# Optimization experiments

Hardware: AMD Instinct MI355X
Metric: run time of the kernel (lower is better)

## Reference

```python
import jax, jax.numpy as jnp
import numpy as np

B, S, E, H = 2, 2048, 2048, 16
D = E // H  # head_dim = 128


def setup_inputs() -> dict:
    key = jax.random.key(0)
    ks = jax.random.split(key, 11)
    scale = 1.0 / np.sqrt(E)
    return {
        "query": jax.random.normal(ks[0], (B, S, E), dtype=jnp.float32),
        "key_in": jax.random.normal(ks[1], (B, S, E), dtype=jnp.float32),
        "value": jax.random.normal(ks[2], (B, S, E), dtype=jnp.float32),
        "Wq": jax.random.normal(ks[3], (E, E), dtype=jnp.float32) * scale,
        "bq": jnp.zeros((E,), dtype=jnp.float32),
        "Wk": jax.random.normal(ks[4], (E, E), dtype=jnp.float32) * scale,
        "bk": jnp.zeros((E,), dtype=jnp.float32),
        "Wv": jax.random.normal(ks[5], (E, E), dtype=jnp.float32) * scale,
        "bv": jnp.zeros((E,), dtype=jnp.float32),
        "Wo": jax.random.normal(ks[6], (E, E), dtype=jnp.float32) * scale,
        "bo": jnp.zeros((E,), dtype=jnp.float32),
    }


def reference(query, key_in, value, Wq, bq, Wk, bk, Wv, bv, Wo, bo):
    # Linear projections then split heads: (B,S,E) -> (B,H,S,D)
    def proj(x, W, b):
        y = x @ W + b
        return y.reshape(B, S, H, D).transpose(0, 2, 1, 3)

    Q = proj(query, Wq, bq)
    K = proj(key_in, Wk, bk)
    V = proj(value, Wv, bv)

    # scores: (B,H,S,S)
    scores = jnp.einsum('bhqd,bhkd->bhqk', Q, K) / jnp.sqrt(jnp.float32(D))
    attn = jax.nn.softmax(scores, axis=-1)
    # attn output: (B,H,S,D) -> (B,S,E)
    out = jnp.einsum('bhqk,bhkd->bhqd', attn, V)
    out = out.transpose(0, 2, 1, 3).reshape(B, S, E)
    return out @ Wo + bo
```

## Files before the change

kernel.cpp:

```cpp
#include <hip/hip_runtime.h>
#include <hip/hip_bf16.h>

typedef __bf16 bf16;
typedef __bf16 bf16x8 __attribute__((ext_vector_type(8)));
typedef float f32x4 __attribute__((ext_vector_type(4)));

constexpr int kE = 2048;
constexpr int kS = 2048;
constexpr int kB = 2;
constexpr int kH = 16;
constexpr int kD = 128;
constexpr int kM = kB * kS;
constexpr float kQScale = 0.12751743f;

#define MFMA_BF16(A, B, C) __builtin_amdgcn_mfma_f32_16x16x32_bf16((A), (B), (C), 0, 0, 0)

__device__ __forceinline__ void async_ld16(const void* gsrc, void* ldst) {
  __builtin_amdgcn_global_load_lds(
      (__attribute__((address_space(1))) void*)(gsrc),
      (__attribute__((address_space(3))) void*)(ldst), 16, 0, 0);
}

__global__ __launch_bounds__(256) void cvt_kernel(
    const float* __restrict__ Xq, const float* __restrict__ Xk,
    const float* __restrict__ Xv, bf16* __restrict__ Y) {
  const int z = blockIdx.y;
  const float* X = (z == 0) ? Xq : (z == 1) ? Xk : Xv;
  bf16* Yz = Y + (size_t)z * kM * kE;
  size_t i = ((size_t)blockIdx.x * 256 + threadIdx.x) * 8;
  float4 v0 = *(const float4*)(X + i);
  float4 v1 = *(const float4*)(X + i + 4);
  bf16x8 hv;
  hv[0] = (bf16)v0.x; hv[1] = (bf16)v0.y; hv[2] = (bf16)v0.z; hv[3] = (bf16)v0.w;
  hv[4] = (bf16)v1.x; hv[5] = (bf16)v1.y; hv[6] = (bf16)v1.z; hv[7] = (bf16)v1.w;
  *(bf16x8*)(Yz + i) = hv;
}

__global__ __launch_bounds__(256) void wt_kernel(
    const float* __restrict__ Wq, const float* __restrict__ Wk,
    const float* __restrict__ Wv, const float* __restrict__ Wo,
    bf16* __restrict__ WT) {
  __shared__ bf16 tl[64][72];
  const int z = blockIdx.z;
  const float* W = (z == 0) ? Wq : (z == 1) ? Wk : (z == 2) ? Wv : Wo;
  const int n0 = blockIdx.x * 64, k0 = blockIdx.y * 64;
  const int t = threadIdx.x;

  {
    const int k = t >> 2, nq = (t & 3) * 16;
    const float* src = &W[(size_t)(k0 + k) * kE + n0 + nq];
#pragma unroll
    for (int u = 0; u < 4; ++u) {
      float4 v = *(const float4*)(src + u * 4);
      tl[nq + u * 4 + 0][k] = (bf16)v.x;
      tl[nq + u * 4 + 1][k] = (bf16)v.y;
      tl[nq + u * 4 + 2][k] = (bf16)v.z;
      tl[nq + u * 4 + 3][k] = (bf16)v.w;
    }
  }
  __syncthreads();
  {
    const int n = t >> 2, seg = (t & 3) * 16;
    bf16x8 a = *(const bf16x8*)&tl[n][seg];
    bf16x8 b2 = *(const bf16x8*)&tl[n][seg + 8];
    bf16* dst = &WT[(size_t)(z * kE + n0 + n) * kE + k0 + seg];
    *(bf16x8*)dst = a;
    *(bf16x8*)(dst + 8) = b2;
  }
}

__global__ __launch_bounds__(256) void gemm_qkv_kernel(
    const bf16* __restrict__ A, const bf16* __restrict__ Bt,
    const float* __restrict__ bias, bf16* __restrict__ dstbuf,
    const float oscale) {
  __shared__ alignas(16) bf16 As[128 * 64];
  __shared__ alignas(16) bf16 Bs[128 * 64];

  const int n0 = blockIdx.x * 128;
  const int m0 = blockIdx.y * 128;
  const int t = threadIdx.x;
  const int lane = t & 63;
  const int w = t >> 6;
  const int ln = lane & 15;
  const int qd = lane >> 4;
  const int wm = w >> 1, wn = w & 1;

  const f32x4 fzero = {0.f, 0.f, 0.f, 0.f};
  f32x4 acc[4][4];
#pragma unroll
  for (int i = 0; i < 4; ++i)
#pragma unroll
    for (int j = 0; j < 4; ++j) acc[i][j] = fzero;

  for (int k0 = 0; k0 < kE; k0 += 64) {
    __syncthreads();
#pragma unroll
    for (int i = 0; i < 4; ++i) {
      int c = t + i * 256;
      int row = c >> 3;
      int slot = c & 7;
      int g = slot ^ (row & 7);
      async_ld16(&A[(size_t)(m0 + row) * kE + k0 + g * 8],
                 &As[(size_t)(w * 64 + i * 256) * 8]);
    }
#pragma unroll
    for (int i = 0; i < 4; ++i) {
      int c = t + i * 256;
      int row = c >> 3;
      int slot = c & 7;
      int g = slot ^ (row & 7);
      async_ld16(&Bt[(size_t)(n0 + row) * kE + k0 + g * 8],
                 &Bs[(size_t)(w * 64 + i * 256) * 8]);
    }
    __syncthreads();
#pragma unroll
    for (int ks = 0; ks < 2; ++ks) {
      bf16x8 af[4], bfv[4];
#pragma unroll
      for (int i = 0; i < 4; ++i) {
        int row = wm * 64 + i * 16 + ln;
        int slot = (ks * 4 + qd) ^ (ln & 7);
        af[i] = *(const bf16x8*)&As[row * 64 + slot * 8];
      }
#pragma unroll
      for (int j = 0; j < 4; ++j) {
        int row = wn * 64 + j * 16 + ln;
        int slot = (ks * 4 + qd) ^ (ln & 7);
        bfv[j] = *(const bf16x8*)&Bs[row * 64 + slot * 8];
      }
#pragma unroll
      for (int i = 0; i < 4; ++i)
#pragma unroll
        for (int j = 0; j < 4; ++j)
          acc[i][j] = MFMA_BF16(af[i], bfv[j], acc[i][j]);
    }
  }

#pragma unroll
  for (int i = 0; i < 4; ++i) {
    int mbase = m0 + wm * 64 + i * 16 + qd * 4;
#pragma unroll
    for (int j = 0; j < 4; ++j) {
      int n = n0 + wn * 64 + j * 16 + ln;
      float bn = bias[n];
      int h = n >> 7, d = n & 127;
#pragma unroll
      for (int r = 0; r < 4; ++r) {
        int mm = mbase + r;
        int bb = mm >> 11, ss = mm & (kS - 1);
        dstbuf[((size_t)(bb * kH + h) * kS + ss) * kD + d] =
            (bf16)((acc[i][j][r] + bn) * oscale);
      }
    }
  }
}

__global__ __launch_bounds__(256) void vtrans_kernel(
    const bf16* __restrict__ Vb, bf16* __restrict__ VT) {
  __shared__ bf16 tl[64][72];
  const int bh = blockIdx.z;
  const int s0 = blockIdx.x * 64, d0 = blockIdx.y * 64;
  const bf16* src = Vb + ((size_t)bh * kS + s0) * kD + d0;
  bf16* dst = VT + ((size_t)bh * kD + d0) * kS + s0;
  const int t = threadIdx.x;
#pragma unroll
  for (int i = 0; i < 2; ++i) {
    int c = t + i * 256;
    int s = c >> 3, dc = (c & 7) * 8;
    bf16x8 v = *(const bf16x8*)&src[(size_t)s * kD + dc];
#pragma unroll
    for (int e = 0; e < 8; ++e) tl[dc + e][s] = v[e];
  }
  __syncthreads();
#pragma unroll
  for (int i = 0; i < 2; ++i) {
    int c = t + i * 256;
    int d = c >> 3, sc = (c & 7) * 8;
    bf16x8 v = *(const bf16x8*)&tl[d][sc];
    *(bf16x8*)&dst[(size_t)d * kS + sc] = v;
  }
}

__global__ __launch_bounds__(256) void attn_kernel(
    const bf16* __restrict__ Qb, const bf16* __restrict__ Kb,
    const bf16* __restrict__ VTb, bf16* __restrict__ AO) {
  __shared__ alignas(16) bf16 Kt[2][64 * 128];
  __shared__ alignas(16) bf16 Vt[2][128 * 64];
  __shared__ alignas(16) bf16 Pl[4][32 * 64];

  const int wg = blockIdx.x;
  const int swz = (wg & 7) * 64 + (wg >> 3);
  const int bh = swz >> 4;
  const int q0 = (swz & 15) * 128;
  const int t = threadIdx.x, lane = t & 63, w = t >> 6;
  const int ln = lane & 15, qd = lane >> 4;

  const bf16* Qh = Qb + (size_t)bh * kS * kD;
  const bf16* Kh = Kb + (size_t)bh * kS * kD;
  const bf16* Vh = VTb + (size_t)bh * kD * kS;

  bf16x8 qf[2][4];
#pragma unroll
  for (int m = 0; m < 2; ++m) {
    int qr = q0 + w * 32 + m * 16 + ln;
#pragma unroll
    for (int f = 0; f < 4; ++f)
      qf[m][f] = *(const bf16x8*)&Qh[(size_t)qr * kD + f * 32 + qd * 8];
  }

  auto stage = [&](int buf, int kc) {
#pragma unroll
    for (int i = 0; i < 4; ++i) {
      int c = t + i * 256;
      int row = c >> 4;
      int slot = c & 15;
      int g = slot ^ (row & 15);
      async_ld16(&Kh[(size_t)(kc + row) * kD + g * 8],
                 &Kt[buf][(size_t)(w * 64 + i * 256) * 8]);
    }
#pragma unroll
    for (int i = 0; i < 4; ++i) {
      int c = t + i * 256;
      int row = c >> 3;
      int slot = c & 7;
      int g = slot ^ (row & 7);
      async_ld16(&Vh[(size_t)row * kS + kc + g * 8],
                 &Vt[buf][(size_t)(w * 64 + i * 256) * 8]);
    }
  };

  const f32x4 fzero = {0.f, 0.f, 0.f, 0.f};
  f32x4 o[2][8];
#pragma unroll
  for (int m = 0; m < 2; ++m)
#pragma unroll
    for (int dt = 0; dt < 8; ++dt) o[m][dt] = fzero;
  float lsum[2][4] = {{0.f, 0.f, 0.f, 0.f}, {0.f, 0.f, 0.f, 0.f}};

  stage(0, 0);

#pragma unroll 1
  for (int u = 0; u < 32; ++u) {
    const int cur = u & 1;
    int knext = (u < 31) ? (u + 1) * 64 : 31 * 64;
    stage(cur ^ 1, knext);
    asm volatile("s_waitcnt vmcnt(8)" ::: "memory");
    __builtin_amdgcn_s_barrier();
    asm volatile("" ::: "memory");

    f32x4 s[2][4];
#pragma unroll
    for (int m = 0; m < 2; ++m)
#pragma unroll
      for (int nt = 0; nt < 4; ++nt) s[m][nt] = fzero;
    __builtin_amdgcn_s_setprio(1);
#pragma unroll
    for (int nt = 0; nt < 4; ++nt) {
      int row = nt * 16 + ln;
#pragma unroll
      for (int f = 0; f < 4; ++f) {
        int slot = (f * 4 + qd) ^ ln;
        bf16x8 kfv = *(const bf16x8*)&Kt[cur][row * 128 + slot * 8];
        s[0][nt] = MFMA_BF16(qf[0][f], kfv, s[0][nt]);
        s[1][nt] = MFMA_BF16(qf[1][f], kfv, s[1][nt]);
      }
    }
    __builtin_amdgcn_s_setprio(0);

#pragma unroll
    for (int m = 0; m < 2; ++m)
#pragma unroll
      for (int nt = 0; nt < 4; ++nt)
#pragma unroll
        for (int r = 0; r < 4; ++r) {
          float p = __builtin_amdgcn_exp2f(s[m][nt][r]);
          lsum[m][r] += p;
          int prow = m * 16 + qd * 4 + r;
          int gchunk = nt * 2 + (ln >> 3);
          int slot = gchunk ^ (prow & 7);
          Pl[w][prow * 64 + slot * 8 + (ln & 7)] = (bf16)p;
        }
    asm volatile("s_waitcnt lgkmcnt(0)" ::: "memory");

    bf16x8 pf[2][2];
#pragma unroll
    for (int m = 0; m < 2; ++m)
#pragma unroll
      for (int kf = 0; kf < 2; ++kf) {
        int slot = (kf * 4 + qd) ^ (ln & 7);
        pf[m][kf] = *(const bf16x8*)&Pl[w][(m * 16 + ln) * 64 + slot * 8];
      }
    __builtin_amdgcn_s_setprio(1);
#pragma unroll
    for (int dt = 0; dt < 8; ++dt) {
      int row = dt * 16 + ln;
#pragma unroll
      for (int kf = 0; kf < 2; ++kf) {
        int slot = (kf * 4 + qd) ^ (ln & 7);
        bf16x8 vv = *(const bf16x8*)&Vt[cur][row * 64 + slot * 8];
        o[0][dt] = MFMA_BF16(pf[0][kf], vv, o[0][dt]);
        o[1][dt] = MFMA_BF16(pf[1][kf], vv, o[1][dt]);
      }
    }
    __builtin_amdgcn_s_setprio(0);

    asm volatile("s_waitcnt lgkmcnt(0)" ::: "memory");
    __builtin_amdgcn_s_barrier();
    asm volatile("" ::: "memory");
  }

#pragma unroll
  for (int m = 0; m < 2; ++m)
#pragma unroll
    for (int r = 0; r < 4; ++r) {
      float l = lsum[m][r];
      l += __shfl_xor(l, 1);
      l += __shfl_xor(l, 2);
      l += __shfl_xor(l, 4);
      l += __shfl_xor(l, 8);
      float inv = 1.f / l;
      int srow = q0 + w * 32 + m * 16 + qd * 4 + r;
      bf16* dst = AO + (size_t)((bh >> 4) * kS + srow) * kE + (bh & 15) * kD;
#pragma unroll
      for (int dt = 0; dt < 8; ++dt)
        dst[dt * 16 + ln] = (bf16)(o[m][dt][r] * inv);
    }
}

__global__ __launch_bounds__(256) void gemm_out_kernel(
    const bf16* __restrict__ A, const bf16* __restrict__ Bt,
    const float* __restrict__ bias, float* __restrict__ out) {
  __shared__ alignas(16) bf16 As[128 * 64];
  __shared__ alignas(16) bf16 Bs[128 * 64];

  const int n0 = blockIdx.x * 128;
  const int m0 = blockIdx.y * 128;
  const int t = threadIdx.x;
  const int lane = t & 63;
  const int w = t >> 6;
  const int ln = lane & 15;
  const int qd = lane >> 4;
  const int wm = w >> 1, wn = w & 1;

  const f32x4 fzero = {0.f, 0.f, 0.f, 0.f};
  f32x4 acc[4][4];
#pragma unroll
  for (int i = 0; i < 4; ++i)
#pragma unroll
    for (int j = 0; j < 4; ++j) acc[i][j] = fzero;

  for (int k0 = 0; k0 < kE; k0 += 64) {
    __syncthreads();
#pragma unroll
    for (int i = 0; i < 4; ++i) {
      int c = t + i * 256;
      int row = c >> 3;
      int slot = c & 7;
      int g = slot ^ (row & 7);
      async_ld16(&A[(size_t)(m0 + row) * kE + k0 + g * 8],
                 &As[(size_t)(w * 64 + i * 256) * 8]);
    }
#pragma unroll
    for (int i = 0; i < 4; ++i) {
      int c = t + i * 256;
      int row = c >> 3;
      int slot = c & 7;
      int g = slot ^ (row & 7);
      async_ld16(&Bt[(size_t)(n0 + row) * kE + k0 + g * 8],
                 &Bs[(size_t)(w * 64 + i * 256) * 8]);
    }
    __syncthreads();
#pragma unroll
    for (int ks = 0; ks < 2; ++ks) {
      bf16x8 af[4], bfv[4];
#pragma unroll
      for (int i = 0; i < 4; ++i) {
        int row = wm * 64 + i * 16 + ln;
        int slot = (ks * 4 + qd) ^ (ln & 7);
        af[i] = *(const bf16x8*)&As[row * 64 + slot * 8];
      }
#pragma unroll
      for (int j = 0; j < 4; ++j) {
        int row = wn * 64 + j * 16 + ln;
        int slot = (ks * 4 + qd) ^ (ln & 7);
        bfv[j] = *(const bf16x8*)&Bs[row * 64 + slot * 8];
      }
#pragma unroll
      for (int i = 0; i < 4; ++i)
#pragma unroll
        for (int j = 0; j < 4; ++j)
          acc[i][j] = MFMA_BF16(af[i], bfv[j], acc[i][j]);
    }
  }

#pragma unroll
  for (int i = 0; i < 4; ++i) {
    int mbase = m0 + wm * 64 + i * 16 + qd * 4;
#pragma unroll
    for (int j = 0; j < 4; ++j) {
      int n = n0 + wn * 64 + j * 16 + ln;
      float bn = bias[n];
#pragma unroll
      for (int r = 0; r < 4; ++r) {
        int mm = mbase + r;
        out[(size_t)mm * kE + n] = acc[i][j][r] + bn;
      }
    }
  }
}

extern "C" void kernel_launch(void* const* d_in, const int* in_sizes, int n_in,
                              void* d_out, int out_size, void* d_ws,
                              size_t ws_size, hipStream_t stream) {
  const float* query  = (const float*)d_in[0];
  const float* key_in = (const float*)d_in[1];
  const float* value  = (const float*)d_in[2];
  const float* Wq = (const float*)d_in[3];
  const float* bq = (const float*)d_in[4];
  const float* Wk = (const float*)d_in[5];
  const float* bk = (const float*)d_in[6];
  const float* Wv = (const float*)d_in[7];
  const float* bv = (const float*)d_in[8];
  const float* Wo = (const float*)d_in[9];
  const float* bo = (const float*)d_in[10];
  float* out = (float*)d_out;

  const size_t szWT  = (size_t)4 * kE * kE;
  const size_t szAct = (size_t)kM * kE;
  const size_t need = (szWT + 7 * szAct) * sizeof(bf16);
  if (ws_size < need) return;

  bf16* WT  = (bf16*)d_ws;
  bf16* Qb  = WT + szWT;
  bf16* Kb  = Qb + szAct;
  bf16* VTb = Kb + szAct;
  bf16* AO  = VTb + szAct;
  bf16* Xb  = AO + szAct;
  bf16* Vb  = AO;

  wt_kernel<<<dim3(kE / 64, kE / 64, 4), 256, 0, stream>>>(
      Wq, Wk, Wv, Wo, WT);
  cvt_kernel<<<dim3(kM * kE / 8 / 256, 3), 256, 0, stream>>>(
      query, key_in, value, Xb);
  gemm_qkv_kernel<<<dim3(kE / 128, kM / 128), 256, 0, stream>>>(
      Xb, WT, bq, Qb, kQScale);
  gemm_qkv_kernel<<<dim3(kE / 128, kM / 128), 256, 0, stream>>>(
      Xb + szAct, WT + (size_t)kE * kE, bk, Kb, 1.0f);
  gemm_qkv_kernel<<<dim3(kE / 128, kM / 128), 256, 0, stream>>>(
      Xb + 2 * szAct, WT + (size_t)2 * kE * kE, bv, Vb, 1.0f);
  vtrans_kernel<<<dim3(kS / 64, kD / 64, kB * kH), 256, 0, stream>>>(
      Vb, VTb);
  attn_kernel<<<dim3(kS * kB * kH / 128), 256, 0, stream>>>(Qb, Kb, VTb, AO);
  gemm_out_kernel<<<dim3(kE / 128, kM / 128), 256, 0, stream>>>(
      AO, WT + (size_t)3 * kE * kE, bo, out);
}
```

Measured before the change: 461.9 us.

## Merge prep kernels, batch QKV GEMMs via grid z, write V transposed directly

Combines the activation conversion and weight transpose into one prep launch, runs the three QKV projection GEMMs as a single launch using blockIdx.z, and has the V projection epilogue store directly into the transposed VT layout with 4-element vector writes, removing the separate vtrans kernel. This cuts launch count, removes a full read/write pass over V, and gives the GEMM a larger grid for better occupancy and tail behavior. In exchange, the VT stores stride by kS between lanes and so are poorly coalesced, and the prep kernel now has divergent block roles.

```diff
diff --git a/kernel.cpp b/kernel.cpp
--- a/kernel.cpp
+++ b/kernel.cpp
@@ -2,6 +2,7 @@
 #include <hip/hip_bf16.h>
 
 typedef __bf16 bf16;
+typedef __bf16 bf16x4 __attribute__((ext_vector_type(4)));
 typedef __bf16 bf16x8 __attribute__((ext_vector_type(8)));
 typedef float f32x4 __attribute__((ext_vector_type(4)));
 
@@ -21,60 +22,71 @@
       (__attribute__((address_space(3))) void*)(ldst), 16, 0, 0);
 }
 
-__global__ __launch_bounds__(256) void cvt_kernel(
+__global__ __launch_bounds__(256) void prep_kernel(
     const float* __restrict__ Xq, const float* __restrict__ Xk,
-    const float* __restrict__ Xv, bf16* __restrict__ Y) {
-  const int z = blockIdx.y;
-  const float* X = (z == 0) ? Xq : (z == 1) ? Xk : Xv;
-  bf16* Yz = Y + (size_t)z * kM * kE;
-  size_t i = ((size_t)blockIdx.x * 256 + threadIdx.x) * 8;
-  float4 v0 = *(const float4*)(X + i);
-  float4 v1 = *(const float4*)(X + i + 4);
-  bf16x8 hv;
-  hv[0] = (bf16)v0.x; hv[1] = (bf16)v0.y; hv[2] = (bf16)v0.z; hv[3] = (bf16)v0.w;
-  hv[4] = (bf16)v1.x; hv[5] = (bf16)v1.y; hv[6] = (bf16)v1.z; hv[7] = (bf16)v1.w;
-  *(bf16x8*)(Yz + i) = hv;
-}
-
-__global__ __launch_bounds__(256) void wt_kernel(
+    const float* __restrict__ Xv, bf16* __restrict__ Y,
     const float* __restrict__ Wq, const float* __restrict__ Wk,
     const float* __restrict__ Wv, const float* __restrict__ Wo,
     bf16* __restrict__ WT) {
   __shared__ bf16 tl[64][72];
-  const int z = blockIdx.z;
-  const float* W = (z == 0) ? Wq : (z == 1) ? Wk : (z == 2) ? Wv : Wo;
-  const int n0 = blockIdx.x * 64, k0 = blockIdx.y * 64;
+  const int blk = blockIdx.x;
   const int t = threadIdx.x;
 
-  {
-    const int k = t >> 2, nq = (t & 3) * 16;
-    const float* src = &W[(size_t)(k0 + k) * kE + n0 + nq];
-#pragma unroll
-    for (int u = 0; u < 4; ++u) {
-      float4 v = *(const float4*)(src + u * 4);
-      tl[nq + u * 4 + 0][k] = (bf16)v.x;
-      tl[nq + u * 4 + 1][k] = (bf16)v.y;
-      tl[nq + u * 4 + 2][k] = (bf16)v.z;
-      tl[nq + u * 4 + 3][k] = (bf16)v.w;
-    }
-  }
-  __syncthreads();
-  {
-    const int n = t >> 2, seg = (t & 3) * 16;
-    bf16x8 a = *(const bf16x8*)&tl[n][seg];
-    bf16x8 b2 = *(const bf16x8*)&tl[n][seg + 8];
-    bf16* dst = &WT[(size_t)(z * kE + n0 + n) * kE + k0 + seg];
-    *(bf16x8*)dst = a;
-    *(bf16x8*)(dst + 8) = b2;
+  if (blk < 12288) {
+    const int z = blk >> 12;
+    const int bx = blk & 4095;
+    const float* X = (z == 0) ? Xq : (z == 1) ? Xk : Xv;
+    bf16* Yz = Y + (size_t)z * kM * kE;
+    size_t i = ((size_t)bx * 256 + t) * 8;
+    float4 v0 = *(const float4*)(X + i);
+    float4 v1 = *(const float4*)(X + i + 4);
+    bf16x8 hv;
+    hv[0] = (bf16)v0.x; hv[1] = (bf16)v0.y; hv[2] = (bf16)v0.z; hv[3] = (bf16)v0.w;
+    hv[4] = (bf16)v1.x; hv[5] = (bf16)v1.y; hv[6] = (bf16)v1.z; hv[7] = (bf16)v1.w;
+    *(bf16x8*)(Yz + i) = hv;
+  } else {
+    const int idx = blk - 12288;
+    const int z = idx >> 10;
+    const int xy = idx & 1023;
+    const int n0 = (xy & 31) * 64, k0 = (xy >> 5) * 64;
+    const float* W = (z == 0) ? Wq : (z == 1) ? Wk : (z == 2) ? Wv : Wo;
+    {
+      const int k = t >> 2, nq = (t & 3) * 16;
+      const float* src = &W[(size_t)(k0 + k) * kE + n0 + nq];
+#pragma unroll
+      for (int u = 0; u < 4; ++u) {
+        float4 v = *(const float4*)(src + u * 4);
+        tl[nq + u * 4 + 0][k] = (bf16)v.x;
+        tl[nq + u * 4 + 1][k] = (bf16)v.y;
+        tl[nq + u * 4 + 2][k] = (bf16)v.z;
+        tl[nq + u * 4 + 3][k] = (bf16)v.w;
+      }
+    }
+    __syncthreads();
+    {
+      const int n = t >> 2, seg = (t & 3) * 16;
+      bf16x8 a = *(const bf16x8*)&tl[n][seg];
+      bf16x8 b2 = *(const bf16x8*)&tl[n][seg + 8];
+      bf16* dst = &WT[(size_t)(z * kE + n0 + n) * kE + k0 + seg];
+      *(bf16x8*)dst = a;
+      *(bf16x8*)(dst + 8) = b2;
+    }
   }
 }
 
 __global__ __launch_bounds__(256) void gemm_qkv_kernel(
-    const bf16* __restrict__ A, const bf16* __restrict__ Bt,
-    const float* __restrict__ bias, bf16* __restrict__ dstbuf,
-    const float oscale) {
+    const bf16* __restrict__ Xb, const bf16* __restrict__ WT,
+    const float* __restrict__ bq, const float* __restrict__ bk,
+    const float* __restrict__ bv, bf16* __restrict__ Qb,
+    bf16* __restrict__ Kb, bf16* __restrict__ VTb) {
   __shared__ alignas(16) bf16 As[128 * 64];
   __shared__ alignas(16) bf16 Bs[128 * 64];
+
+  const int z = blockIdx.z;
+  const bf16* A = Xb + (size_t)z * kM * kE;
+  const float* bias = (z == 0) ? bq : (z == 1) ? bk : bv;
+  const float oscale = (z == 0) ? kQScale : 1.0f;
+  const bf16* Bt = WT + (size_t)z * kE * kE;
 
   const int n0 = blockIdx.x * 128;
   const int m0 = blockIdx.y * 128;
@@ -136,48 +148,41 @@
     }
   }
 
-#pragma unroll
-  for (int i = 0; i < 4; ++i) {
-    int mbase = m0 + wm * 64 + i * 16 + qd * 4;
-#pragma unroll
-    for (int j = 0; j < 4; ++j) {
-      int n = n0 + wn * 64 + j * 16 + ln;
-      float bn = bias[n];
-      int h = n >> 7, d = n & 127;
-#pragma unroll
-      for (int r = 0; r < 4; ++r) {
-        int mm = mbase + r;
-        int bb = mm >> 11, ss = mm & (kS - 1);
-        dstbuf[((size_t)(bb * kH + h) * kS + ss) * kD + d] =
-            (bf16)((acc[i][j][r] + bn) * oscale);
-      }
-    }
-  }
-}
-
-__global__ __launch_bounds__(256) void vtrans_kernel(
-    const bf16* __restrict__ Vb, bf16* __restrict__ VT) {
-  __shared__ bf16 tl[64][72];
-  const int bh = blockIdx.z;
-  const int s0 = blockIdx.x * 64, d0 = blockIdx.y * 64;
-  const bf16* src = Vb + ((size_t)bh * kS + s0) * kD + d0;
-  bf16* dst = VT + ((size_t)bh * kD + d0) * kS + s0;
-  const int t = threadIdx.x;
-#pragma unroll
-  for (int i = 0; i < 2; ++i) {
-    int c = t + i * 256;
-    int s = c >> 3, dc = (c & 7) * 8;
-    bf16x8 v = *(const bf16x8*)&src[(size_t)s * kD + dc];
-#pragma unroll
-    for (int e = 0; e < 8; ++e) tl[dc + e][s] = v[e];
-  }
-  __syncthreads();
-#pragma unroll
-  for (int i = 0; i < 2; ++i) {
-    int c = t + i * 256;
-    int d = c >> 3, sc = (c & 7) * 8;
-    bf16x8 v = *(const bf16x8*)&tl[d][sc];
-    *(bf16x8*)&dst[(size_t)d * kS + sc] = v;
+  if (z != 2) {
+    bf16* dstbuf = (z == 0) ? Qb : Kb;
+#pragma unroll
+    for (int i = 0; i < 4; ++i) {
+      int mbase = m0 + wm * 64 + i * 16 + qd * 4;
+#pragma unroll
+      for (int j = 0; j < 4; ++j) {
+        int n = n0 + wn * 64 + j * 16 + ln;
+        float bn = bias[n];
+        int h = n >> 7, d = n & 127;
+#pragma unroll
+        for (int r = 0; r < 4; ++r) {
+          int mm = mbase + r;
+          int bb = mm >> 11, ss = mm & (kS - 1);
+          dstbuf[((size_t)(bb * kH + h) * kS + ss) * kD + d] =
+              (bf16)((acc[i][j][r] + bn) * oscale);
+        }
+      }
+    }
+  } else {
+#pragma unroll
+    for (int i = 0; i < 4; ++i) {
+      int mbase = m0 + wm * 64 + i * 16 + qd * 4;
+      int bb = mbase >> 11, ss0 = mbase & (kS - 1);
+#pragma unroll
+      for (int j = 0; j < 4; ++j) {
+        int n = n0 + wn * 64 + j * 16 + ln;
+        float bn = bias[n];
+        int h = n >> 7, d = n & 127;
+        bf16x4 v;
+#pragma unroll
+        for (int r = 0; r < 4; ++r) v[r] = (bf16)(acc[i][j][r] + bn);
+        *(bf16x4*)&VTb[((size_t)(bb * kH + h) * kD + d) * kS + ss0] = v;
+      }
+    }
   }
 }
 
@@ -436,20 +441,11 @@
   bf16* VTb = Kb + szAct;
   bf16* AO  = VTb + szAct;
   bf16* Xb  = AO + szAct;
-  bf16* Vb  = AO;
-
-  wt_kernel<<<dim3(kE / 64, kE / 64, 4), 256, 0, stream>>>(
-      Wq, Wk, Wv, Wo, WT);
-  cvt_kernel<<<dim3(kM * kE / 8 / 256, 3), 256, 0, stream>>>(
-      query, key_in, value, Xb);
-  gemm_qkv_kernel<<<dim3(kE / 128, kM / 128), 256, 0, stream>>>(
-      Xb, WT, bq, Qb, kQScale);
-  gemm_qkv_kernel<<<dim3(kE / 128, kM / 128), 256, 0, stream>>>(
-      Xb + szAct, WT + (size_t)kE * kE, bk, Kb, 1.0f);
-  gemm_qkv_kernel<<<dim3(kE / 128, kM / 128), 256, 0, stream>>>(
-      Xb + 2 * szAct, WT + (size_t)2 * kE * kE, bv, Vb, 1.0f);
-  vtrans_kernel<<<dim3(kS / 64, kD / 64, kB * kH), 256, 0, stream>>>(
-      Vb, VTb);
+
+  prep_kernel<<<dim3(12288 + 4096), 256, 0, stream>>>(
+      query, key_in, value, Xb, Wq, Wk, Wv, Wo, WT);
+  gemm_qkv_kernel<<<dim3(kE / 128, kM / 128, 3), 256, 0, stream>>>(
+      Xb, WT, bq, bk, bv, Qb, Kb, VTb);
   attn_kernel<<<dim3(kS * kB * kH / 128), 256, 0, stream>>>(Qb, Kb, VTb, AO);
   gemm_out_kernel<<<dim3(kE / 128, kM / 128), 256, 0, stream>>>(
       AO, WT + (size_t)3 * kE * kE, bo, out);
```

After: 438.9 us. -5.0%, faster.
